# Optimization experiments

Measured on AMD Instinct MI355X. Metric: run time of the kernel, lower is better.

## Reference

```python
import jax, jax.numpy as jnp
import numpy as np

N_EMBED = 1024
HEAD_SIZE = 64
BLOCK_SIZE = 2048


def setup_inputs() -> dict:
    key = jax.random.key(0)
    kx, kk, kv = jax.random.split(key, 3)
    x = jax.random.normal(kx, (8, 2048, N_EMBED), dtype=jnp.float32)
    # nn.Linear(n_embed, head_size, bias=False): weight [head_size, n_embed]
    scale = 1.0 / np.sqrt(N_EMBED)
    W_k = jax.random.uniform(kk, (HEAD_SIZE, N_EMBED), dtype=jnp.float32, minval=-scale, maxval=scale)
    W_v = jax.random.uniform(kv, (HEAD_SIZE, N_EMBED), dtype=jnp.float32, minval=-scale, maxval=scale)
    return {"x": x, "W_k": W_k, "W_v": W_v}


def reference(x, W_k, W_v):
    # Faithful to source: q = self.key(x) (query projection is unused in the original forward)
    T = x.shape[1]
    k = jnp.einsum('btc,hc->bth', x, W_k)   # [B,T,H]
    q = k                                    # source bug: q uses key projection
    wei = jnp.einsum('bth,bsh->bts', q, k) * (HEAD_SIZE ** -0.5)  # [B,T,T]
    causal = jnp.tril(jnp.ones((T, T), dtype=bool))
    wei = jnp.where(causal, wei, -jnp.inf)
    wei = jax.nn.softmax(wei, axis=-1)
    v = jnp.einsum('btc,hc->bth', x, W_v)
    out = jnp.einsum('bts,bsh->bth', wei, v)
    return out
```

## Files before the change

kernel.cpp:

```cpp
#include <hip/hip_runtime.h>


typedef __bf16 bf16;
typedef __bf16 bf16x4 __attribute__((ext_vector_type(4)));
typedef __bf16 bf16x8 __attribute__((ext_vector_type(8)));
typedef float  floatx4 __attribute__((ext_vector_type(4)));

#define T_LEN 2048
#define HEAD  64
#define CEMB  1024

static __device__ __forceinline__ bf16x8 cvt2(float4 a, float4 b) {
    bf16x8 r;
    r[0] = (bf16)a.x; r[1] = (bf16)a.y; r[2] = (bf16)a.z; r[3] = (bf16)a.w;
    r[4] = (bf16)b.x; r[5] = (bf16)b.y; r[6] = (bf16)b.z; r[7] = (bf16)b.w;
    return r;
}

static __device__ __forceinline__ void gload_lds16(const void* g, void* l) {
    __builtin_amdgcn_global_load_lds(
        (const __attribute__((address_space(1))) unsigned int*)(unsigned long long)g,
        (__attribute__((address_space(3))) unsigned int*)(unsigned long long)l,
        16, 0, 0);
}

__global__ __launch_bounds__(256) void wconv_kernel(const float* __restrict__ Wk,
                                                    const float* __restrict__ Wv,
                                                    bf16* __restrict__ Wb) {
    int i = (blockIdx.x * 256 + threadIdx.x) * 4;
    const float* src = (i < 64 * 1024) ? (Wk + i) : (Wv + (i - 64 * 1024));
    float4 f = *(const float4*)src;
    bf16x4 v;
    v[0] = (bf16)f.x; v[1] = (bf16)f.y; v[2] = (bf16)f.z; v[3] = (bf16)f.w;
    *(bf16x4*)&Wb[i] = v;
}

__global__ __launch_bounds__(256) void proj_kernel(const float* __restrict__ x,
                                                   const bf16* __restrict__ Wb,
                                                   bf16* __restrict__ Kbuf,
                                                   bf16* __restrict__ Vt) {
    __shared__ __align__(16) bf16 As[2][32][72];
    __shared__ __align__(16) bf16 Bs[2][128][64];

    const int tid  = threadIdx.x;
    const int wave = tid >> 6;
    const int lane = tid & 63;
    const int quad = lane >> 4;
    const int low  = lane & 15;

    const long row0 = (long)blockIdx.x * 32;

    const int a_row = tid >> 3;
    const int a_col = (tid & 7) * 8;
    const float* abase = x + (row0 + a_row) * CEMB + a_col;

    const int brow = tid >> 3;
    const int cbp  = (tid & 7) * 16;
    const int bsw  = cbp ^ ((brow & 7) << 4);
    const char* bsrc0 = (const char*)Wb + (long)brow * (CEMB * 2) + bsw;
    char* bdst = (char*)&Bs[0][0][0] + wave * 1024;

    const int strip = wave & 1;
    const int nhalf = wave >> 1;
    const int nq    = nhalf * 4;

    floatx4 acc[4];
#pragma unroll
    for (int i = 0; i < 4; ++i) acc[i] = (floatx4){0.f, 0.f, 0.f, 0.f};

    float4 apf[2][2];

    apf[0][0] = ((const float4*)abase)[0];
    apf[0][1] = ((const float4*)abase)[1];
#pragma unroll
    for (int r = 0; r < 4; ++r)
        gload_lds16(bsrc0 + (long)r * 65536, bdst + r * 4096);
    *(bf16x8*)&As[0][a_row][a_col] = cvt2(apf[0][0], apf[0][1]);
    apf[1][0] = ((const float4*)(abase + 64))[0];
    apf[1][1] = ((const float4*)(abase + 64))[1];
    __syncthreads();

    const int bswz = (low & 7) << 4;
    int buf = 0;
    for (int s = 0; s < 16; ++s) {
        if (s < 15) {
            const int q  = (s + 1) & 1;
            const int nb = buf ^ 1;
            *(bf16x8*)&As[nb][a_row][a_col] = cvt2(apf[q][0], apf[q][1]);
#pragma unroll
            for (int r = 0; r < 4; ++r)
                gload_lds16(bsrc0 + (long)r * 65536 + (s + 1) * 128,
                            bdst + nb * 16384 + r * 4096);
        }
        if (s < 14) {
            const int q  = s & 1;
            const int k0 = (s + 2) * 64;
            apf[q][0] = ((const float4*)(abase + k0))[0];
            apf[q][1] = ((const float4*)(abase + k0))[1];
        }
        const char* bsl = (const char*)&Bs[buf][0][0];
#pragma unroll
        for (int ks = 0; ks < 2; ++ks) {
            bf16x8 afrag = *(const bf16x8*)&As[buf][strip * 16 + low][ks * 32 + quad * 8];
            const int cb = (ks * 64 + quad * 16) ^ bswz;
#pragma unroll
            for (int i = 0; i < 4; ++i) {
                bf16x8 bfrag = *(const bf16x8*)(bsl + ((nq + i) * 16 + low) * 128 + cb);
                acc[i] = __builtin_amdgcn_mfma_f32_16x16x32_bf16(afrag, bfrag, acc[i], 0, 0, 0);
            }
        }
        if (s < 15) {
            __syncthreads();
            buf ^= 1;
        }
    }

    __syncthreads();
    bf16* Ek = (bf16*)&Bs[0][0][0];
    bf16* Ev = (bf16*)&Bs[1][0][0];
    if (nhalf == 0) {
#pragma unroll
        for (int i = 0; i < 4; ++i)
#pragma unroll
            for (int r = 0; r < 4; ++r)
                Ek[(strip * 16 + quad * 4 + r) * 72 + i * 16 + low] = (bf16)acc[i][r];
    } else {
#pragma unroll
        for (int i = 0; i < 4; ++i)
#pragma unroll
            for (int r = 0; r < 4; ++r)
                Ev[(i * 16 + low) * 36 + strip * 16 + quad * 4 + r] = (bf16)acc[i][r];
    }
    __syncthreads();

    const long bidx  = row0 >> 11;
    const int  tloc0 = (int)(row0 & 2047);
    {
        const int t  = tid >> 3;
        const int h0 = (tid & 7) * 8;
        *(bf16x8*)&Kbuf[(bidx * T_LEN + tloc0 + t) * HEAD + h0] = *(const bf16x8*)&Ek[t * 72 + h0];
    }
    {
        const int h  = tid >> 2;
        const int t0 = (tid & 3) * 8;
        *(bf16x8*)&Vt[(bidx * HEAD + h) * T_LEN + tloc0 + t0] = *(const bf16x8*)&Ev[h * 36 + t0];
    }
}

__global__ __launch_bounds__(256) void attn_kernel(const bf16* __restrict__ Kbuf,
                                                   const bf16* __restrict__ Vt,
                                                   bf16* __restrict__ Opart,
                                                   float* __restrict__ lpart) {
    __shared__ __align__(16) bf16 Ks[2][64][64];
    __shared__ __align__(16) bf16 Vs[2][64][64];
    __shared__ __align__(16) bf16 Ps[4][16][72];

    const int tid  = threadIdx.x;
    const int wave = tid >> 6;
    const int lane = tid & 63;
    const int quad = lane >> 4;
    const int low  = lane & 15;

    const int c  = blockIdx.x & 3;
    const int qb = (blockIdx.x >> 2) & 31;
    const int b  = blockIdx.x >> 7;

    const bf16* kbase = Kbuf + (long)b * T_LEN * HEAD;
    const bf16* vbase = Vt + (long)b * HEAD * T_LEN;

    const bf16* qrow = kbase + (qb * 64 + wave * 16 + low) * HEAD + quad * 8;
    const bf16x8 qf0 = *(const bf16x8*)(qrow);
    const bf16x8 qf1 = *(const bf16x8*)(qrow + 32);

    bf16x8 ones;
#pragma unroll
    for (int i = 0; i < 8; ++i) ones[i] = (bf16)1.0f;

    floatx4 o[4], ol;
#pragma unroll
    for (int nt = 0; nt < 4; ++nt) o[nt] = (floatx4){0.f, 0.f, 0.f, 0.f};
    ol = (floatx4){0.f, 0.f, 0.f, 0.f};

    const int srow = tid >> 3;
    const int cbp  = (tid & 7) * 16;
    const int ssw  = cbp ^ ((srow & 7) << 4);
    const char* ksrc0 = (const char*)kbase + (long)srow * 128  + ssw;
    const char* vsrc0 = (const char*)vbase + (long)srow * 4096 + ssw;
    char* kdst = (char*)&Ks[0][0][0] + wave * 1024;
    char* vdst = (char*)&Vs[0][0][0] + wave * 1024;

    const int sw  = (low & 7) << 4;
    const int cb0 = (quad * 16) ^ sw;
    const int cb1 = (64 + quad * 16) ^ sw;

    if (c <= qb) {
#pragma unroll
        for (int r = 0; r < 2; ++r) {
            gload_lds16(ksrc0 + (long)c * 8192 + r * 4096, kdst + r * 4096);
            gload_lds16(vsrc0 + (long)c * 128 + (long)r * 131072, vdst + r * 4096);
        }
        __syncthreads();

        int buf = 0;
        for (int j = c; j <= qb; j += 4) {
            const bool more = (j + 4 <= qb);
            if (more) {
                const int nb = buf ^ 1;
#pragma unroll
                for (int r = 0; r < 2; ++r) {
                    gload_lds16(ksrc0 + (long)(j + 4) * 8192 + r * 4096,
                                kdst + nb * 8192 + r * 4096);
                    gload_lds16(vsrc0 + (long)(j + 4) * 128 + (long)r * 131072,
                                vdst + nb * 8192 + r * 4096);
                }
            }
            const char* ksl = (const char*)&Ks[buf][0][0];
            const char* vsl = (const char*)&Vs[buf][0][0];

            floatx4 s_[4];
#pragma unroll
            for (int nt = 0; nt < 4; ++nt) {
                bf16x8 kf0 = *(const bf16x8*)(ksl + (nt * 16 + low) * 128 + cb0);
                bf16x8 kf1 = *(const bf16x8*)(ksl + (nt * 16 + low) * 128 + cb1);
                floatx4 z = (floatx4){0.f, 0.f, 0.f, 0.f};
                z = __builtin_amdgcn_mfma_f32_16x16x32_bf16(qf0, kf0, z, 0, 0, 0);
                z = __builtin_amdgcn_mfma_f32_16x16x32_bf16(qf1, kf1, z, 0, 0, 0);
                s_[nt] = z;
            }

            const bool diag = (j == qb);
#pragma unroll
            for (int nt = 0; nt < 4; ++nt) {
#pragma unroll
                for (int r = 0; r < 4; ++r) {
                    float p = __builtin_amdgcn_exp2f(s_[nt][r] * 0.180336880f);
                    if (diag && (nt * 16 + low) > (wave * 16 + quad * 4 + r)) p = 0.f;
                    Ps[wave][quad * 4 + r][nt * 16 + low] = (bf16)p;
                }
            }

            bf16x8 pf0 = *(const bf16x8*)&Ps[wave][low][quad * 8];
            bf16x8 pf1 = *(const bf16x8*)&Ps[wave][low][32 + quad * 8];
#pragma unroll
            for (int nt = 0; nt < 4; ++nt) {
                bf16x8 vf0 = *(const bf16x8*)(vsl + (nt * 16 + low) * 128 + cb0);
                bf16x8 vf1 = *(const bf16x8*)(vsl + (nt * 16 + low) * 128 + cb1);
                o[nt] = __builtin_amdgcn_mfma_f32_16x16x32_bf16(pf0, vf0, o[nt], 0, 0, 0);
                o[nt] = __builtin_amdgcn_mfma_f32_16x16x32_bf16(pf1, vf1, o[nt], 0, 0, 0);
            }
            ol = __builtin_amdgcn_mfma_f32_16x16x32_bf16(pf0, ones, ol, 0, 0, 0);
            ol = __builtin_amdgcn_mfma_f32_16x16x32_bf16(pf1, ones, ol, 0, 0, 0);

            if (more) {
                __syncthreads();
                buf ^= 1;
            }
        }
    }

    __syncthreads();
    bf16* Eo = (bf16*)&Ks[0][0][0];
#pragma unroll
    for (int nt = 0; nt < 4; ++nt)
#pragma unroll
        for (int r = 0; r < 4; ++r)
            Eo[(wave * 16 + quad * 4 + r) * 72 + nt * 16 + low] = (bf16)o[nt][r];
    __syncthreads();
    {
        const int row  = tid >> 2;
        const int col0 = (tid & 3) * 16;
        bf16* ob = Opart + (long)blockIdx.x * 4096 + row * 64 + col0;
        *(bf16x8*)(ob)     = *(const bf16x8*)&Eo[row * 72 + col0];
        *(bf16x8*)(ob + 8) = *(const bf16x8*)&Eo[row * 72 + col0 + 8];
    }
    if (low == 0) {
#pragma unroll
        for (int r = 0; r < 4; ++r)
            lpart[(long)blockIdx.x * 64 + wave * 16 + quad * 4 + r] = ol[r];
    }
}

__global__ __launch_bounds__(256) void attn_combine(const bf16* __restrict__ Opart,
                                                    const float* __restrict__ lpart,
                                                    float* __restrict__ out) {
    const int tile = blockIdx.x >> 2;
    const int rg   = blockIdx.x & 3;
    const int tid  = threadIdx.x;
    const int row  = rg * 16 + (tid >> 4);
    const int col0 = (tid & 15) * 4;

    const bf16*  ob = Opart + (long)tile * 4 * 4096 + row * 64 + col0;
    const float* lb = lpart + (long)tile * 4 * 64 + row;

    float l = lb[0] + lb[64] + lb[128] + lb[192];
    float rl = 1.0f / l;

    float s[4] = {0.f, 0.f, 0.f, 0.f};
#pragma unroll
    for (int ch = 0; ch < 4; ++ch) {
        bf16x4 u = *(const bf16x4*)(ob + ch * 4096);
#pragma unroll
        for (int i = 0; i < 4; ++i) s[i] += (float)u[i];
    }
    float4 w;
    w.x = s[0] * rl; w.y = s[1] * rl; w.z = s[2] * rl; w.w = s[3] * rl;
    *(float4*)(out + (long)tile * 4096 + row * 64 + col0) = w;
}

extern "C" void kernel_launch(void* const* d_in, const int* in_sizes, int n_in,
                              void* d_out, int out_size, void* d_ws, size_t ws_size,
                              hipStream_t stream) {
    const float* x  = (const float*)d_in[0];
    const float* Wk = (const float*)d_in[1];
    const float* Wv = (const float*)d_in[2];
    float* out = (float*)d_out;

    char* ws = (char*)d_ws;
    bf16*  Wb    = (bf16*)ws;
    bf16*  Kbuf  = (bf16*)(ws + (1 << 20));
    bf16*  Vt    = (bf16*)(ws + (3 << 20));
    bf16*  Opart = (bf16*)(ws + (5 << 20));
    float* lpart = (float*)(ws + (13 << 20));

    wconv_kernel<<<128, 256, 0, stream>>>(Wk, Wv, Wb);
    proj_kernel<<<512, 256, 0, stream>>>(x, Wb, Kbuf, Vt);
    attn_kernel<<<1024, 256, 0, stream>>>(Kbuf, Vt, Opart, lpart);
    attn_combine<<<1024, 256, 0, stream>>>(Opart, lpart, out);
}
```

Measured before the change: 128.3 us.

## Load projection A fragments straight into registers and raise MFMA wave priority

The projection kernel no longer stages x tiles through shared memory. Each lane loads its own MFMA A-fragment from global fp32, double-buffered in registers, and converts it to bf16 just before use. This removes the LDS write/read for A and sets an occupancy hint via launch_bounds(256,4). The attention kernel wraps its MFMA sections in s_setprio so matrix-issuing waves get scheduling priority. The cost is less coalesced global loads for x (16 rows × 32B per wave) and more registers used for prefetch.

```diff
diff --git a/kernel.cpp b/kernel.cpp
--- a/kernel.cpp
+++ b/kernel.cpp
@@ -35,11 +35,10 @@
     *(bf16x4*)&Wb[i] = v;
 }
 
-__global__ __launch_bounds__(256) void proj_kernel(const float* __restrict__ x,
-                                                   const bf16* __restrict__ Wb,
-                                                   bf16* __restrict__ Kbuf,
-                                                   bf16* __restrict__ Vt) {
-    __shared__ __align__(16) bf16 As[2][32][72];
+__global__ __launch_bounds__(256, 4) void proj_kernel(const float* __restrict__ x,
+                                                      const bf16* __restrict__ Wb,
+                                                      bf16* __restrict__ Kbuf,
+                                                      bf16* __restrict__ Vt) {
     __shared__ __align__(16) bf16 Bs[2][128][64];
 
     const int tid  = threadIdx.x;
@@ -50,9 +49,11 @@
 
     const long row0 = (long)blockIdx.x * 32;
 
-    const int a_row = tid >> 3;
-    const int a_col = (tid & 7) * 8;
-    const float* abase = x + (row0 + a_row) * CEMB + a_col;
+    const int strip = wave & 1;
+    const int nhalf = wave >> 1;
+    const int nq    = nhalf * 4;
+
+    const float* afp = x + (row0 + strip * 16 + low) * CEMB + quad * 8;
 
     const int brow = tid >> 3;
     const int cbp  = (tid & 7) * 16;
@@ -60,48 +61,43 @@
     const char* bsrc0 = (const char*)Wb + (long)brow * (CEMB * 2) + bsw;
     char* bdst = (char*)&Bs[0][0][0] + wave * 1024;
 
-    const int strip = wave & 1;
-    const int nhalf = wave >> 1;
-    const int nq    = nhalf * 4;
-
     floatx4 acc[4];
 #pragma unroll
     for (int i = 0; i < 4; ++i) acc[i] = (floatx4){0.f, 0.f, 0.f, 0.f};
 
-    float4 apf[2][2];
-
-    apf[0][0] = ((const float4*)abase)[0];
-    apf[0][1] = ((const float4*)abase)[1];
+    float4 apf[2][2][2];
+
 #pragma unroll
     for (int r = 0; r < 4; ++r)
         gload_lds16(bsrc0 + (long)r * 65536, bdst + r * 4096);
-    *(bf16x8*)&As[0][a_row][a_col] = cvt2(apf[0][0], apf[0][1]);
-    apf[1][0] = ((const float4*)(abase + 64))[0];
-    apf[1][1] = ((const float4*)(abase + 64))[1];
+#pragma unroll
+    for (int ks = 0; ks < 2; ++ks) {
+        apf[0][ks][0] = ((const float4*)(afp + ks * 32))[0];
+        apf[0][ks][1] = ((const float4*)(afp + ks * 32))[1];
+    }
     __syncthreads();
 
     const int bswz = (low & 7) << 4;
     int buf = 0;
     for (int s = 0; s < 16; ++s) {
+        const int cur = s & 1;
         if (s < 15) {
-            const int q  = (s + 1) & 1;
-            const int nb = buf ^ 1;
-            *(bf16x8*)&As[nb][a_row][a_col] = cvt2(apf[q][0], apf[q][1]);
+            const int nb  = buf ^ 1;
+            const int nxt = cur ^ 1;
 #pragma unroll
             for (int r = 0; r < 4; ++r)
                 gload_lds16(bsrc0 + (long)r * 65536 + (s + 1) * 128,
                             bdst + nb * 16384 + r * 4096);
-        }
-        if (s < 14) {
-            const int q  = s & 1;
-            const int k0 = (s + 2) * 64;
-            apf[q][0] = ((const float4*)(abase + k0))[0];
-            apf[q][1] = ((const float4*)(abase + k0))[1];
+#pragma unroll
+            for (int ks = 0; ks < 2; ++ks) {
+                apf[nxt][ks][0] = ((const float4*)(afp + (s + 1) * 64 + ks * 32))[0];
+                apf[nxt][ks][1] = ((const float4*)(afp + (s + 1) * 64 + ks * 32))[1];
+            }
         }
         const char* bsl = (const char*)&Bs[buf][0][0];
 #pragma unroll
         for (int ks = 0; ks < 2; ++ks) {
-            bf16x8 afrag = *(const bf16x8*)&As[buf][strip * 16 + low][ks * 32 + quad * 8];
+            bf16x8 afrag = cvt2(apf[cur][ks][0], apf[cur][ks][1]);
             const int cb = (ks * 64 + quad * 16) ^ bswz;
 #pragma unroll
             for (int i = 0; i < 4; ++i) {
@@ -218,6 +214,7 @@
             const char* vsl = (const char*)&Vs[buf][0][0];
 
             floatx4 s_[4];
+            __builtin_amdgcn_s_setprio(1);
 #pragma unroll
             for (int nt = 0; nt < 4; ++nt) {
                 bf16x8 kf0 = *(const bf16x8*)(ksl + (nt * 16 + low) * 128 + cb0);
@@ -227,6 +224,7 @@
                 z = __builtin_amdgcn_mfma_f32_16x16x32_bf16(qf1, kf1, z, 0, 0, 0);
                 s_[nt] = z;
             }
+            __builtin_amdgcn_s_setprio(0);
 
             const bool diag = (j == qb);
 #pragma unroll
@@ -241,6 +239,7 @@
 
             bf16x8 pf0 = *(const bf16x8*)&Ps[wave][low][quad * 8];
             bf16x8 pf1 = *(const bf16x8*)&Ps[wave][low][32 + quad * 8];
+            __builtin_amdgcn_s_setprio(1);
 #pragma unroll
             for (int nt = 0; nt < 4; ++nt) {
                 bf16x8 vf0 = *(const bf16x8*)(vsl + (nt * 16 + low) * 128 + cb0);
@@ -250,6 +249,7 @@
             }
             ol = __builtin_amdgcn_mfma_f32_16x16x32_bf16(pf0, ones, ol, 0, 0, 0);
             ol = __builtin_amdgcn_mfma_f32_16x16x32_bf16(pf1, ones, ol, 0, 0, 0);
+            __builtin_amdgcn_s_setprio(0);
 
             if (more) {
                 __syncthreads();
```

After: 135.3 us. +5.5%, slower.

## Read K/V fragments directly from global memory instead of LDS double buffering

Applied to the files above, without the earlier changes.

Removes the shared-memory K and V double buffers, the async global-to-LDS loads and the per-iteration block barriers. Each wave now loads its MFMA operand fragments for K and transposed V straight from global memory, and the output staging area reuses the P scratch buffer. This cuts LDS footprint and synchronisation and may raise occupancy. In exchange, all four waves fetch the same tiles redundantly through the caches, the loads are no longer prefetched ahead of compute, and the V reads are strided.

```diff
diff --git a/kernel.cpp b/kernel.cpp
--- a/kernel.cpp
+++ b/kernel.cpp
@@ -151,8 +151,6 @@
                                                    const bf16* __restrict__ Vt,
                                                    bf16* __restrict__ Opart,
                                                    float* __restrict__ lpart) {
-    __shared__ __align__(16) bf16 Ks[2][64][64];
-    __shared__ __align__(16) bf16 Vs[2][64][64];
     __shared__ __align__(16) bf16 Ps[4][16][72];
 
     const int tid  = threadIdx.x;
@@ -181,47 +179,17 @@
     for (int nt = 0; nt < 4; ++nt) o[nt] = (floatx4){0.f, 0.f, 0.f, 0.f};
     ol = (floatx4){0.f, 0.f, 0.f, 0.f};
 
-    const int srow = tid >> 3;
-    const int cbp  = (tid & 7) * 16;
-    const int ssw  = cbp ^ ((srow & 7) << 4);
-    const char* ksrc0 = (const char*)kbase + (long)srow * 128  + ssw;
-    const char* vsrc0 = (const char*)vbase + (long)srow * 4096 + ssw;
-    char* kdst = (char*)&Ks[0][0][0] + wave * 1024;
-    char* vdst = (char*)&Vs[0][0][0] + wave * 1024;
-
-    const int sw  = (low & 7) << 4;
-    const int cb0 = (quad * 16) ^ sw;
-    const int cb1 = (64 + quad * 16) ^ sw;
-
     if (c <= qb) {
-#pragma unroll
-        for (int r = 0; r < 2; ++r) {
-            gload_lds16(ksrc0 + (long)c * 8192 + r * 4096, kdst + r * 4096);
-            gload_lds16(vsrc0 + (long)c * 128 + (long)r * 131072, vdst + r * 4096);
-        }
-        __syncthreads();
-
-        int buf = 0;
         for (int j = c; j <= qb; j += 4) {
-            const bool more = (j + 4 <= qb);
-            if (more) {
-                const int nb = buf ^ 1;
-#pragma unroll
-                for (int r = 0; r < 2; ++r) {
-                    gload_lds16(ksrc0 + (long)(j + 4) * 8192 + r * 4096,
-                                kdst + nb * 8192 + r * 4096);
-                    gload_lds16(vsrc0 + (long)(j + 4) * 128 + (long)r * 131072,
-                                vdst + nb * 8192 + r * 4096);
-                }
-            }
-            const char* ksl = (const char*)&Ks[buf][0][0];
-            const char* vsl = (const char*)&Vs[buf][0][0];
+            const bf16* ktile = kbase + (long)(j * 64) * HEAD;
+            const bf16* vtile = vbase + j * 64;
 
             floatx4 s_[4];
 #pragma unroll
             for (int nt = 0; nt < 4; ++nt) {
-                bf16x8 kf0 = *(const bf16x8*)(ksl + (nt * 16 + low) * 128 + cb0);
-                bf16x8 kf1 = *(const bf16x8*)(ksl + (nt * 16 + low) * 128 + cb1);
+                const bf16* kr = ktile + (nt * 16 + low) * HEAD + quad * 8;
+                bf16x8 kf0 = *(const bf16x8*)(kr);
+                bf16x8 kf1 = *(const bf16x8*)(kr + 32);
                 floatx4 z = (floatx4){0.f, 0.f, 0.f, 0.f};
                 z = __builtin_amdgcn_mfma_f32_16x16x32_bf16(qf0, kf0, z, 0, 0, 0);
                 z = __builtin_amdgcn_mfma_f32_16x16x32_bf16(qf1, kf1, z, 0, 0, 0);
@@ -243,23 +211,19 @@
             bf16x8 pf1 = *(const bf16x8*)&Ps[wave][low][32 + quad * 8];
 #pragma unroll
             for (int nt = 0; nt < 4; ++nt) {
-                bf16x8 vf0 = *(const bf16x8*)(vsl + (nt * 16 + low) * 128 + cb0);
-                bf16x8 vf1 = *(const bf16x8*)(vsl + (nt * 16 + low) * 128 + cb1);
+                const bf16* vr = vtile + (long)(nt * 16 + low) * T_LEN + quad * 8;
+                bf16x8 vf0 = *(const bf16x8*)(vr);
+                bf16x8 vf1 = *(const bf16x8*)(vr + 32);
                 o[nt] = __builtin_amdgcn_mfma_f32_16x16x32_bf16(pf0, vf0, o[nt], 0, 0, 0);
                 o[nt] = __builtin_amdgcn_mfma_f32_16x16x32_bf16(pf1, vf1, o[nt], 0, 0, 0);
             }
             ol = __builtin_amdgcn_mfma_f32_16x16x32_bf16(pf0, ones, ol, 0, 0, 0);
             ol = __builtin_amdgcn_mfma_f32_16x16x32_bf16(pf1, ones, ol, 0, 0, 0);
-
-            if (more) {
-                __syncthreads();
-                buf ^= 1;
-            }
-        }
-    }
-
-    __syncthreads();
-    bf16* Eo = (bf16*)&Ks[0][0][0];
+        }
+    }
+
+    __syncthreads();
+    bf16* Eo = (bf16*)&Ps[0][0][0];
 #pragma unroll
     for (int nt = 0; nt < 4; ++nt)
 #pragma unroll
```

New measurement: 170.2 us. 1.33x slower.
